# Kernel optimization log

Hardware: AMD Instinct MI355X
Metric: run time of the kernel (lower is better)

The kernel has to match this reference:

```python
import jax, jax.numpy as jnp
import numpy as np

# Config mirroring My_MLP(mlp_layers=2, isize=512, k=30, non_linearity='relu',
#                        mlp_act='relu', offset_list=[2048]*4)
SIZES = [2048, 2048, 2048, 2048]   # per-client subgraph sizes (offset_list)
N = sum(SIZES)                      # 8192 total nodes
D = 512                             # isize
K = 30 + 1                          # module uses self.k + 1


def setup_inputs() -> dict:
    key = jax.random.key(0)
    k1, k2, k3 = jax.random.split(key, 3)
    features = jax.random.normal(k1, (N, D), dtype=jnp.float32)
    # Diag layer weights: a learned diagonal (vector) per layer, init near 1.
    w0 = 1.0 + 0.1 * jax.random.normal(k2, (D,), dtype=jnp.float32)
    w1 = 1.0 + 0.1 * jax.random.normal(k3, (D,), dtype=jnp.float32)
    return {"features": features, "w0": w0, "w1": w1}


def reference(features, w0, w1):
    # internal_forward: Diag -> relu -> Diag (no act after last layer)
    h = jax.nn.relu(features * w0) * w1                 # [N, D]
    # F.normalize(dim=1, p=2)
    emb = h * jax.lax.rsqrt(jnp.sum(h * h, axis=1, keepdims=True) + 1e-24)
    sim = jnp.matmul(emb, emb.T)                        # [N, N]

    # cross_subgraph_topk: per row, keep top-(k+1) similarities among columns
    # belonging to a DIFFERENT client subgraph; zero everything else.
    seg = jnp.asarray(np.repeat(np.arange(len(SIZES)), SIZES))   # [N] int
    same = seg[:, None] == seg[None, :]                           # [N, N] bool
    masked = jnp.where(same, -jnp.inf, sim)
    vals, inds = jax.lax.top_k(masked, K)                         # [N, K]
    rows = jnp.arange(N)[:, None]
    out = jnp.zeros_like(sim).at[rows, inds].set(vals)

    # apply_non_linearity('relu', i)
    return jax.nn.relu(out)
```

## Files before the change

kernel.cpp:

```cpp
#include <hip/hip_runtime.h>
#include <hip/hip_bf16.h>
#include <hip/hip_fp16.h>
#include <math.h>

typedef unsigned short u16;
typedef unsigned int u32;
typedef unsigned long long u64;
typedef __attribute__((ext_vector_type(8))) short bf16x8;
typedef __attribute__((ext_vector_type(4))) float f32x4;

#define N_NODES 8192
#define DIM 512
#define KSEL 31
#define BANDCAP 128
#define SEG_SIZE 2048
#define NVALID 6144
#define BAND_ULP 8

__device__ __forceinline__ u32 f16key(u32 h) {
  return (h & 0x8000u) ? (0xFFFFu & ~h) : (h | 0x8000u);
}
__device__ __forceinline__ u32 packkeys(u32 w) {
  return f16key(w & 0xFFFFu) | (f16key(w >> 16) << 16);
}
__device__ __forceinline__ float keyval(u32 k) {
  const u16 raw = (k & 0x8000u) ? (u16)(k ^ 0x8000u) : (u16)(~k & 0xFFFFu);
  __half_raw hr; hr.x = raw;
  return __half2float(__half(hr));
}

#define GLD_LDS16(g, l)                                        \
  __builtin_amdgcn_global_load_lds(                            \
      (const __attribute__((address_space(1))) void*)(g),      \
      (__attribute__((address_space(3))) void*)(l), 16, 0, 0)

__global__ __launch_bounds__(256) void prep_kernel(
    const float* __restrict__ feat, const float* __restrict__ w0,
    const float* __restrict__ w1, u16* __restrict__ embh,
    float* __restrict__ embf, u32* __restrict__ kmax32) {
#pragma clang fp contract(off)
  const int row = blockIdx.x;
  const int t = threadIdx.x;
  __shared__ float hs[DIM];
  __shared__ float partial[32];
  __shared__ float rinv_sh;

  const float2 x = *reinterpret_cast<const float2*>(feat + (size_t)row * DIM + t * 2);
  const float2 a = *reinterpret_cast<const float2*>(w0 + t * 2);
  const float2 b = *reinterpret_cast<const float2*>(w1 + t * 2);
  const float h0 = fmaxf(x.x * a.x, 0.0f) * b.x;
  const float h1 = fmaxf(x.y * a.y, 0.0f) * b.y;
  hs[t * 2] = h0;
  hs[t * 2 + 1] = h1;
  if (t == 0) kmax32[row] = 0u;
  __syncthreads();

  if (t < 32) {
    const int base = (t >> 3) * 128 + (t & 7);
    float v = hs[base];
    float acc = v * v;
    for (int i = 1; i < 16; ++i) {
      v = hs[base + 8 * i];
      const float vv = v * v;
      acc = acc + vv;
    }
    partial[t] = acc;
  }
  __syncthreads();
  if (t == 0) {
    float B[4];
    for (int blk = 0; blk < 4; ++blk) {
      const float* p = &partial[blk * 8];
      B[blk] = ((p[0] + p[1]) + (p[2] + p[3])) + ((p[4] + p[5]) + (p[6] + p[7]));
    }
    const float s = (B[0] + B[1]) + (B[2] + B[3]);
    const float sp = s + 1e-24f;
    const float qf = (float)sqrt((double)sp);
    rinv_sh = (float)(1.0 / (double)qf);
  }
  __syncthreads();
  const float rinv = rinv_sh;
  const float e0 = h0 * rinv;
  const float e1 = h1 * rinv;
  *reinterpret_cast<float2*>(embf + (size_t)row * DIM + t * 2) = make_float2(e0, e1);
  __hip_bfloat162 bb;
  bb.x = __float2bfloat16(e0);
  bb.y = __float2bfloat16(e1);
  *reinterpret_cast<__hip_bfloat162*>(embh + (size_t)row * DIM + t * 2) = bb;
}

__global__ __launch_bounds__(256) void gemm_kernel(const u16* __restrict__ embh,
                                                   __half* __restrict__ simh,
                                                   u32* __restrict__ kmax32) {
  __shared__ u16 As[128][64];
  __shared__ u16 Bs[128][64];
  const int tid = threadIdx.x;
  const int lane = tid & 63;
  const int wave = tid >> 6;
  const int wm = wave >> 1;
  const int wn = wave & 1;
  const int rowTile = blockIdx.y;
  const int segTileBase = (rowTile >> 4) << 4;
  const int cT = blockIdx.x;
  const int colTile = cT < segTileBase ? cT : cT + 16;
  const int row0 = rowTile * 128;
  const int col0 = colTile * 128;

  f32x4 acc[4][4] = {};

  for (int k0 = 0; k0 < DIM; k0 += 64) {
#pragma unroll
    for (int i = 0; i < 4; ++i) {
      const int flat = i * 256 + tid;
      const int r = flat >> 3;
      const int c = (flat & 7) * 8;
      GLD_LDS16(embh + (size_t)(row0 + r) * DIM + k0 + c, &As[r][c]);
      GLD_LDS16(embh + (size_t)(col0 + r) * DIM + k0 + c, &Bs[r][c]);
    }
    __syncthreads();
#pragma unroll
    for (int kk = 0; kk < 2; ++kk) {
      bf16x8 afr[4], bfr[4];
      const int koff = kk * 32 + (lane >> 4) * 8;
      const int rsel = lane & 15;
#pragma unroll
      for (int m = 0; m < 4; ++m)
        afr[m] = *reinterpret_cast<const bf16x8*>(&As[wm * 64 + m * 16 + rsel][koff]);
#pragma unroll
      for (int n = 0; n < 4; ++n)
        bfr[n] = *reinterpret_cast<const bf16x8*>(&Bs[wn * 64 + n * 16 + rsel][koff]);
#pragma unroll
      for (int m = 0; m < 4; ++m)
#pragma unroll
        for (int n = 0; n < 4; ++n)
          acc[m][n] = __builtin_amdgcn_mfma_f32_16x16x32_bf16(afr[m], bfr[n],
                                                              acc[m][n], 0, 0, 0);
    }
    __syncthreads();
  }
#pragma unroll
  for (int m = 0; m < 4; ++m)
#pragma unroll
    for (int n = 0; n < 4; ++n)
#pragma unroll
      for (int j = 0; j < 4; ++j) {
        const int r = row0 + wm * 64 + m * 16 + (lane >> 4) * 4 + j;
        const int pcol = cT * 128 + wn * 64 + n * 16 + (lane & 15);
        simh[(size_t)r * NVALID + pcol] = __float2half(acc[m][n][j]);
      }
#pragma unroll
  for (int m = 0; m < 4; ++m) {
#pragma unroll
    for (int j = 0; j < 4; ++j) {
      float vmax = fmaxf(fmaxf(acc[m][0][j], acc[m][1][j]),
                         fmaxf(acc[m][2][j], acc[m][3][j]));
#pragma unroll
      for (int off = 1; off < 16; off <<= 1)
        vmax = fmaxf(vmax, __shfl_xor(vmax, off, 64));
      if ((lane & 15) == 0) {
        const int r = row0 + wm * 64 + m * 16 + (lane >> 4) * 4 + j;
        const u32 b = __float_as_uint(vmax);
        const u32 kk = (b & 0x80000000u) ? ~b : (b | 0x80000000u);
        atomicMax(&kmax32[r], kk);
      }
    }
  }
}

__global__ __launch_bounds__(256) void select_kernel(
    const __half* __restrict__ simh, const float* __restrict__ embf,
    const u32* __restrict__ kmax32, int2* __restrict__ compact) {
  const int row = blockIdx.x;
  const int t = threadIdx.x;
  const int lane = t & 63;
  const int wave = t >> 6;

  __shared__ u32 hist[257];
  __shared__ int bcol[BANDCAP];
  __shared__ float bex[BANDCAP];
  __shared__ int outidx_s[KSEL];
  __shared__ float outval_s[KSEL];
  __shared__ int cnts[2];
  __shared__ u32 sh_lo, sh_hi, sh_need;
  __shared__ int sh_state;

  const int segBase = (row >> 11) << 11;

  u32 pk[12];
  {
    const uint4* src = reinterpret_cast<const uint4*>(simh + (size_t)row * NVALID);
    const uint4 a = src[t], b = src[256 + t], c = src[512 + t];
    pk[0] = packkeys(a.x); pk[1] = packkeys(a.y);
    pk[2] = packkeys(a.z); pk[3] = packkeys(a.w);
    pk[4] = packkeys(b.x); pk[5] = packkeys(b.y);
    pk[6] = packkeys(b.z); pk[7] = packkeys(b.w);
    pk[8] = packkeys(c.x); pk[9] = packkeys(c.y);
    pk[10] = packkeys(c.z); pk[11] = packkeys(c.w);
  }
#define KEY(v) ((pk[(v) >> 1] >> (((v) & 1) * 16)) & 0xFFFFu)
#define COL(v) ((((((v) >> 3) * 256) + t) << 3) + ((v) & 7))

  if (t < KSEL) { outidx_s[t] = segBase; outval_s[t] = 0.0f; }
  if (t == 0) { cnts[0] = 0; cnts[1] = 0; }

  u32 kmax16;
  {
    const u32 kk = kmax32[row];
    const u32 fb = (kk & 0x80000000u) ? (kk ^ 0x80000000u) : ~kk;
    const __half h = __float2half(__uint_as_float(fb));
    kmax16 = f16key((u32)__half_as_ushort(h));
  }

  u32 base = (kmax16 > 511u) ? kmax16 - 511u : 0u;
  u32 winTop = kmax16;
  u32 shift = 2;
  u32 need = KSEL;
  int tier = 0;
  for (int guard = 0; guard < 6; ++guard) {
    hist[t] = 0;
    if (t == 0) hist[256] = 0;
    __syncthreads();
#pragma unroll
    for (int v = 0; v < 24; ++v) {
      const u32 k = KEY(v);
      if (k >= base && k <= winTop) atomicAdd(&hist[(k - base) >> shift], 1u);
    }
    __syncthreads();
    if (wave == 0) {
      const int x = lane * 4;
      const u32 b0 = hist[x], b1 = hist[x + 1];
      const u32 b2 = hist[x + 2], b3 = hist[x + 3];
      const u32 tot = b0 + b1 + b2 + b3;
      u32 inc = tot;
#pragma unroll
      for (int off = 1; off < 64; off <<= 1) {
        const u32 vv = (u32)__shfl_down((int)inc, off, 64);
        if (lane + off < 64) inc += vv;
      }
      const u32 exc = inc - tot;
      const u32 g3 = exc, g2 = g3 + b3, g1 = g2 + b2, g0 = g1 + b1;
      int sel = -1;
      u32 gsel = 0;
      if (g3 < need && g3 + b3 >= need) { sel = x + 3; gsel = g3; }
      else if (g2 < need && g2 + b2 >= need) { sel = x + 2; gsel = g2; }
      else if (g1 < need && g1 + b1 >= need) { sel = x + 1; gsel = g1; }
      else if (g0 < need && g0 + b0 >= need) { sel = x;     gsel = g0; }
      const u64 bal = __ballot(sel >= 0);
      if (lane == 0 && bal == 0) sh_state = 0;
      if (bal != 0) {
        const int srcl = (int)(__ffsll((unsigned long long)bal) - 1);
        sel  = __shfl(sel, srcl, 64);
        gsel = (u32)__shfl((int)gsel, srcl, 64);
        if (lane == 0) {
          const u32 blo = base + ((u32)sel << shift);
          const u32 bhi = min(blo + (1u << shift) - 1u, winTop);
          sh_lo = blo; sh_hi = bhi; sh_need = need - gsel;
          sh_state = (shift > 2) ? 1 : 2;
        }
      }
    }
    __syncthreads();
    const int st = sh_state;
    if (st == 2) break;
    if (st == 1) {
      base = sh_lo; winTop = sh_hi; shift = 0; need = sh_need;
    } else {
      ++tier;
      if (tier == 1) { base = (kmax16 > 8191u) ? kmax16 - 8191u : 0u; shift = 5; }
      else { base = 0u; shift = 8; }
      winTop = kmax16; need = KSEL;
    }
    __syncthreads();
  }
  const u32 binlo = sh_lo, binhi = sh_hi;
  const u32 hiK = binhi + BAND_ULP;
  const u32 loK = (binlo >= BAND_ULP) ? binlo - BAND_ULP : 0u;

#pragma unroll
  for (int v = 0; v < 24; ++v) {
    const u32 k = KEY(v);
    if (k > hiK) {
      const int slot = atomicAdd(&cnts[1], 1);
      const int i = COL(v);
      if (slot < KSEL) {
        outidx_s[slot] = (i < segBase) ? i : i + SEG_SIZE;
        outval_s[slot] = fmaxf(keyval(k), 0.0f);
      }
    } else if (k >= loK) {
      const int slot = atomicAdd(&cnts[0], 1);
      const int i = COL(v);
      if (slot < BANDCAP) bcol[slot] = (i < segBase) ? i : i + SEG_SIZE;
    }
  }
  __syncthreads();
  const int nH = min(cnts[1], KSEL);
  const int slots = KSEL - nH;
  const int nB = min(cnts[0], BANDCAP);

  if (t < nB) {
#pragma clang fp contract(off)
    const float4* g4 =
        reinterpret_cast<const float4*>(embf + (size_t)bcol[t] * DIM);
    const float4* e4 = reinterpret_cast<const float4*>(embf + (size_t)row * DIM);
    float acc = 0.0f;
    for (int k4 = 0; k4 < DIM / 4; ++k4) {
      const float4 a = e4[k4];
      const float4 b = g4[k4];
      acc = acc + a.x * b.x;
      acc = acc + a.y * b.y;
      acc = acc + a.z * b.z;
      acc = acc + a.w * b.w;
    }
    bex[t] = acc;
  }
  __syncthreads();

  if (t < nB) {
    const float ev = bex[t];
    const int ec = bcol[t];
    int r = 0;
    for (int j = 0; j < nB; ++j) {
      const float oj = bex[j];
      const int cj = bcol[j];
      if (oj > ev || (oj == ev && cj < ec)) r++;
    }
    if (r < slots) {
      const int slot = atomicAdd(&cnts[1], 1);
      if (slot < KSEL) { outidx_s[slot] = ec; outval_s[slot] = fmaxf(ev, 0.0f); }
    }
  }
  __syncthreads();
  if (t < KSEL)
    compact[(size_t)row * KSEL + t] =
        make_int2(outidx_s[t], __float_as_int(outval_s[t]));
#undef KEY
#undef COL
}

__global__ __launch_bounds__(256) void write_kernel(
    const int2* __restrict__ compact, float* __restrict__ out) {
  const int row = blockIdx.x;
  const int t = threadIdx.x;
  __shared__ int sidx[KSEL];
  __shared__ float sval[KSEL];
  if (t < KSEL) {
    const int2 e = compact[(size_t)row * KSEL + t];
    sidx[t] = e.x;
    sval[t] = __int_as_float(e.y);
  }
  float* orow = out + (size_t)row * N_NODES;
  const float4 zero4 = make_float4(0.f, 0.f, 0.f, 0.f);
  __syncthreads();
#pragma unroll
  for (int i = 0; i < 8; ++i)
    reinterpret_cast<float4*>(orow)[i * 256 + t] = zero4;
  __syncthreads();
  if (t < KSEL) orow[sidx[t]] = sval[t];
}

extern "C" void kernel_launch(void* const* d_in, const int* in_sizes, int n_in,
                              void* d_out, int out_size, void* d_ws, size_t ws_size,
                              hipStream_t stream) {
  const float* feat = (const float*)d_in[0];
  const float* w0 = (const float*)d_in[1];
  const float* w1 = (const float*)d_in[2];
  float* out = (float*)d_out;

  u16* embh = (u16*)d_ws;
  float* embf = (float*)((char*)d_ws + (size_t)N_NODES * DIM * 2);
  u32* kmax32 = (u32*)((char*)d_ws + (size_t)24 * 1024 * 1024);
  int2* compact = (int2*)d_ws;
  __half* simh = (__half*)d_out;

  prep_kernel<<<N_NODES, 256, 0, stream>>>(feat, w0, w1, embh, embf, kmax32);
  dim3 grid(48, 64);
  gemm_kernel<<<grid, 256, 0, stream>>>(embh, simh, kmax32);
  select_kernel<<<N_NODES, 256, 0, stream>>>(simh, embf, kmax32, compact);
  write_kernel<<<N_NODES, 256, 0, stream>>>(compact, out);
}
```

Baseline: 246.3 us.

## Fuse top-k selection with output write using workspace for fp16 similarity

The fp16 similarity matrix moves out of the output buffer into the workspace when the workspace is large enough. Selection can then zero and scatter the output rows directly, so the separate write kernel and the compact buffer round trip are no longer needed. Each select block now handles four rows in sequence, giving 2048 blocks instead of 8192. This depends on the workspace size at run time and falls back to the old two-kernel path otherwise. Fewer blocks may reduce latency hiding in the histogram and selection phases.

After: 265.4 us. 1.08x slower.

```diff
diff --git a/kernel.cpp b/kernel.cpp
--- a/kernel.cpp
+++ b/kernel.cpp
@@ -167,10 +167,11 @@
   }
 }
 
+template <bool FUSED>
 __global__ __launch_bounds__(256) void select_kernel(
     const __half* __restrict__ simh, const float* __restrict__ embf,
-    const u32* __restrict__ kmax32, int2* __restrict__ compact) {
-  const int row = blockIdx.x;
+    const u32* __restrict__ kmax32, int2* __restrict__ compact,
+    float* __restrict__ out) {
   const int t = threadIdx.x;
   const int lane = t & 63;
   const int wave = t >> 6;
@@ -184,157 +185,172 @@
   __shared__ u32 sh_lo, sh_hi, sh_need;
   __shared__ int sh_state;
 
-  const int segBase = (row >> 11) << 11;
-
-  u32 pk[12];
-  {
-    const uint4* src = reinterpret_cast<const uint4*>(simh + (size_t)row * NVALID);
-    const uint4 a = src[t], b = src[256 + t], c = src[512 + t];
-    pk[0] = packkeys(a.x); pk[1] = packkeys(a.y);
-    pk[2] = packkeys(a.z); pk[3] = packkeys(a.w);
-    pk[4] = packkeys(b.x); pk[5] = packkeys(b.y);
-    pk[6] = packkeys(b.z); pk[7] = packkeys(b.w);
-    pk[8] = packkeys(c.x); pk[9] = packkeys(c.y);
-    pk[10] = packkeys(c.z); pk[11] = packkeys(c.w);
-  }
+  for (int rr = 0; rr < 4; ++rr) {
+    const int row = blockIdx.x * 4 + rr;
+    const int segBase = (row >> 11) << 11;
+
+    u32 pk[12];
+    {
+      const uint4* src = reinterpret_cast<const uint4*>(simh + (size_t)row * NVALID);
+      const uint4 a = src[t], b = src[256 + t], c = src[512 + t];
+      pk[0] = packkeys(a.x); pk[1] = packkeys(a.y);
+      pk[2] = packkeys(a.z); pk[3] = packkeys(a.w);
+      pk[4] = packkeys(b.x); pk[5] = packkeys(b.y);
+      pk[6] = packkeys(b.z); pk[7] = packkeys(b.w);
+      pk[8] = packkeys(c.x); pk[9] = packkeys(c.y);
+      pk[10] = packkeys(c.z); pk[11] = packkeys(c.w);
+    }
 #define KEY(v) ((pk[(v) >> 1] >> (((v) & 1) * 16)) & 0xFFFFu)
 #define COL(v) ((((((v) >> 3) * 256) + t) << 3) + ((v) & 7))
 
-  if (t < KSEL) { outidx_s[t] = segBase; outval_s[t] = 0.0f; }
-  if (t == 0) { cnts[0] = 0; cnts[1] = 0; }
-
-  u32 kmax16;
-  {
-    const u32 kk = kmax32[row];
-    const u32 fb = (kk & 0x80000000u) ? (kk ^ 0x80000000u) : ~kk;
-    const __half h = __float2half(__uint_as_float(fb));
-    kmax16 = f16key((u32)__half_as_ushort(h));
-  }
-
-  u32 base = (kmax16 > 511u) ? kmax16 - 511u : 0u;
-  u32 winTop = kmax16;
-  u32 shift = 2;
-  u32 need = KSEL;
-  int tier = 0;
-  for (int guard = 0; guard < 6; ++guard) {
-    hist[t] = 0;
-    if (t == 0) hist[256] = 0;
-    __syncthreads();
+    if (t < KSEL) { outidx_s[t] = segBase; outval_s[t] = 0.0f; }
+    if (t == 0) { cnts[0] = 0; cnts[1] = 0; }
+
+    u32 kmax16;
+    {
+      const u32 kk = kmax32[row];
+      const u32 fb = (kk & 0x80000000u) ? (kk ^ 0x80000000u) : ~kk;
+      const __half h = __float2half(__uint_as_float(fb));
+      kmax16 = f16key((u32)__half_as_ushort(h));
+    }
+
+    u32 base = (kmax16 > 511u) ? kmax16 - 511u : 0u;
+    u32 winTop = kmax16;
+    u32 shift = 2;
+    u32 need = KSEL;
+    int tier = 0;
+    for (int guard = 0; guard < 6; ++guard) {
+      hist[t] = 0;
+      if (t == 0) hist[256] = 0;
+      __syncthreads();
+#pragma unroll
+      for (int v = 0; v < 24; ++v) {
+        const u32 k = KEY(v);
+        if (k >= base && k <= winTop) atomicAdd(&hist[(k - base) >> shift], 1u);
+      }
+      __syncthreads();
+      if (wave == 0) {
+        const int x = lane * 4;
+        const u32 b0 = hist[x], b1 = hist[x + 1];
+        const u32 b2 = hist[x + 2], b3 = hist[x + 3];
+        const u32 tot = b0 + b1 + b2 + b3;
+        u32 inc = tot;
+#pragma unroll
+        for (int off = 1; off < 64; off <<= 1) {
+          const u32 vv = (u32)__shfl_down((int)inc, off, 64);
+          if (lane + off < 64) inc += vv;
+        }
+        const u32 exc = inc - tot;
+        const u32 g3 = exc, g2 = g3 + b3, g1 = g2 + b2, g0 = g1 + b1;
+        int sel = -1;
+        u32 gsel = 0;
+        if (g3 < need && g3 + b3 >= need) { sel = x + 3; gsel = g3; }
+        else if (g2 < need && g2 + b2 >= need) { sel = x + 2; gsel = g2; }
+        else if (g1 < need && g1 + b1 >= need) { sel = x + 1; gsel = g1; }
+        else if (g0 < need && g0 + b0 >= need) { sel = x;     gsel = g0; }
+        const u64 bal = __ballot(sel >= 0);
+        if (lane == 0 && bal == 0) sh_state = 0;
+        if (bal != 0) {
+          const int srcl = (int)(__ffsll((unsigned long long)bal) - 1);
+          sel  = __shfl(sel, srcl, 64);
+          gsel = (u32)__shfl((int)gsel, srcl, 64);
+          if (lane == 0) {
+            const u32 blo = base + ((u32)sel << shift);
+            const u32 bhi = min(blo + (1u << shift) - 1u, winTop);
+            sh_lo = blo; sh_hi = bhi; sh_need = need - gsel;
+            sh_state = (shift > 2) ? 1 : 2;
+          }
+        }
+      }
+      __syncthreads();
+      const int st = sh_state;
+      if (st == 2) break;
+      if (st == 1) {
+        base = sh_lo; winTop = sh_hi; shift = 0; need = sh_need;
+      } else {
+        ++tier;
+        if (tier == 1) { base = (kmax16 > 8191u) ? kmax16 - 8191u : 0u; shift = 5; }
+        else { base = 0u; shift = 8; }
+        winTop = kmax16; need = KSEL;
+      }
+      __syncthreads();
+    }
+    const u32 binlo = sh_lo, binhi = sh_hi;
+    const u32 hiK = binhi + BAND_ULP;
+    const u32 loK = (binlo >= BAND_ULP) ? binlo - BAND_ULP : 0u;
+
 #pragma unroll
     for (int v = 0; v < 24; ++v) {
       const u32 k = KEY(v);
-      if (k >= base && k <= winTop) atomicAdd(&hist[(k - base) >> shift], 1u);
-    }
-    __syncthreads();
-    if (wave == 0) {
-      const int x = lane * 4;
-      const u32 b0 = hist[x], b1 = hist[x + 1];
-      const u32 b2 = hist[x + 2], b3 = hist[x + 3];
-      const u32 tot = b0 + b1 + b2 + b3;
-      u32 inc = tot;
-#pragma unroll
-      for (int off = 1; off < 64; off <<= 1) {
-        const u32 vv = (u32)__shfl_down((int)inc, off, 64);
-        if (lane + off < 64) inc += vv;
-      }
-      const u32 exc = inc - tot;
-      const u32 g3 = exc, g2 = g3 + b3, g1 = g2 + b2, g0 = g1 + b1;
-      int sel = -1;
-      u32 gsel = 0;
-      if (g3 < need && g3 + b3 >= need) { sel = x + 3; gsel = g3; }
-      else if (g2 < need && g2 + b2 >= need) { sel = x + 2; gsel = g2; }
-      else if (g1 < need && g1 + b1 >= need) { sel = x + 1; gsel = g1; }
-      else if (g0 < need && g0 + b0 >= need) { sel = x;     gsel = g0; }
-      const u64 bal = __ballot(sel >= 0);
-      if (lane == 0 && bal == 0) sh_state = 0;
-      if (bal != 0) {
-        const int srcl = (int)(__ffsll((unsigned long long)bal) - 1);
-        sel  = __shfl(sel, srcl, 64);
-        gsel = (u32)__shfl((int)gsel, srcl, 64);
-        if (lane == 0) {
-          const u32 blo = base + ((u32)sel << shift);
-          const u32 bhi = min(blo + (1u << shift) - 1u, winTop);
-          sh_lo = blo; sh_hi = bhi; sh_need = need - gsel;
-          sh_state = (shift > 2) ? 1 : 2;
+      if (k > hiK) {
+        const int slot = atomicAdd(&cnts[1], 1);
+        const int i = COL(v);
+        if (slot < KSEL) {
+          outidx_s[slot] = (i < segBase) ? i : i + SEG_SIZE;
+          outval_s[slot] = fmaxf(keyval(k), 0.0f);
         }
-      }
-    }
-    __syncthreads();
-    const int st = sh_state;
-    if (st == 2) break;
-    if (st == 1) {
-      base = sh_lo; winTop = sh_hi; shift = 0; need = sh_need;
+      } else if (k >= loK) {
+        const int slot = atomicAdd(&cnts[0], 1);
+        const int i = COL(v);
+        if (slot < BANDCAP) bcol[slot] = (i < segBase) ? i : i + SEG_SIZE;
+      }
+    }
+    __syncthreads();
+    const int nH = min(cnts[1], KSEL);
+    const int slots = KSEL - nH;
+    const int nB = min(cnts[0], BANDCAP);
+
+    if (t < nB) {
+#pragma clang fp contract(off)
+      const float4* g4 =
+          reinterpret_cast<const float4*>(embf + (size_t)bcol[t] * DIM);
+      const float4* e4 = reinterpret_cast<const float4*>(embf + (size_t)row * DIM);
+      float acc = 0.0f;
+      for (int k4 = 0; k4 < DIM / 4; ++k4) {
+        const float4 a = e4[k4];
+        const float4 b = g4[k4];
+        acc = acc + a.x * b.x;
+        acc = acc + a.y * b.y;
+        acc = acc + a.z * b.z;
+        acc = acc + a.w * b.w;
+      }
+      bex[t] = acc;
+    }
+    __syncthreads();
+
+    if (t < nB) {
+      const float ev = bex[t];
+      const int ec = bcol[t];
+      int r = 0;
+      for (int j = 0; j < nB; ++j) {
+        const float oj = bex[j];
+        const int cj = bcol[j];
+        if (oj > ev || (oj == ev && cj < ec)) r++;
+      }
+      if (r < slots) {
+        const int slot = atomicAdd(&cnts[1], 1);
+        if (slot < KSEL) { outidx_s[slot] = ec; outval_s[slot] = fmaxf(ev, 0.0f); }
+      }
+    }
+    __syncthreads();
+
+    if constexpr (FUSED) {
+      float* orow = out + (size_t)row * N_NODES;
+      const float4 zero4 = make_float4(0.f, 0.f, 0.f, 0.f);
+#pragma unroll
+      for (int i = 0; i < 8; ++i)
+        reinterpret_cast<float4*>(orow)[i * 256 + t] = zero4;
+      __syncthreads();
+      if (t < KSEL) orow[outidx_s[t]] = outval_s[t];
     } else {
-      ++tier;
-      if (tier == 1) { base = (kmax16 > 8191u) ? kmax16 - 8191u : 0u; shift = 5; }
-      else { base = 0u; shift = 8; }
-      winTop = kmax16; need = KSEL;
-    }
-    __syncthreads();
-  }
-  const u32 binlo = sh_lo, binhi = sh_hi;
-  const u32 hiK = binhi + BAND_ULP;
-  const u32 loK = (binlo >= BAND_ULP) ? binlo - BAND_ULP : 0u;
-
-#pragma unroll
-  for (int v = 0; v < 24; ++v) {
-    const u32 k = KEY(v);
-    if (k > hiK) {
-      const int slot = atomicAdd(&cnts[1], 1);
-      const int i = COL(v);
-      if (slot < KSEL) {
-        outidx_s[slot] = (i < segBase) ? i : i + SEG_SIZE;
-        outval_s[slot] = fmaxf(keyval(k), 0.0f);
-      }
-    } else if (k >= loK) {
-      const int slot = atomicAdd(&cnts[0], 1);
-      const int i = COL(v);
-      if (slot < BANDCAP) bcol[slot] = (i < segBase) ? i : i + SEG_SIZE;
-    }
-  }
-  __syncthreads();
-  const int nH = min(cnts[1], KSEL);
-  const int slots = KSEL - nH;
-  const int nB = min(cnts[0], BANDCAP);
-
-  if (t < nB) {
-#pragma clang fp contract(off)
-    const float4* g4 =
-        reinterpret_cast<const float4*>(embf + (size_t)bcol[t] * DIM);
-    const float4* e4 = reinterpret_cast<const float4*>(embf + (size_t)row * DIM);
-    float acc = 0.0f;
-    for (int k4 = 0; k4 < DIM / 4; ++k4) {
-      const float4 a = e4[k4];
-      const float4 b = g4[k4];
-      acc = acc + a.x * b.x;
-      acc = acc + a.y * b.y;
-      acc = acc + a.z * b.z;
-      acc = acc + a.w * b.w;
-    }
-    bex[t] = acc;
-  }
-  __syncthreads();
-
-  if (t < nB) {
-    const float ev = bex[t];
-    const int ec = bcol[t];
-    int r = 0;
-    for (int j = 0; j < nB; ++j) {
-      const float oj = bex[j];
-      const int cj = bcol[j];
-      if (oj > ev || (oj == ev && cj < ec)) r++;
-    }
-    if (r < slots) {
-      const int slot = atomicAdd(&cnts[1], 1);
-      if (slot < KSEL) { outidx_s[slot] = ec; outval_s[slot] = fmaxf(ev, 0.0f); }
-    }
-  }
-  __syncthreads();
-  if (t < KSEL)
-    compact[(size_t)row * KSEL + t] =
-        make_int2(outidx_s[t], __float_as_int(outval_s[t]));
+      if (t < KSEL)
+        compact[(size_t)row * KSEL + t] =
+            make_int2(outidx_s[t], __float_as_int(outval_s[t]));
+    }
+    __syncthreads();
 #undef KEY
 #undef COL
+  }
 }
 
 __global__ __launch_bounds__(256) void write_kernel(
@@ -370,11 +386,21 @@
   float* embf = (float*)((char*)d_ws + (size_t)N_NODES * DIM * 2);
   u32* kmax32 = (u32*)((char*)d_ws + (size_t)24 * 1024 * 1024);
   int2* compact = (int2*)d_ws;
-  __half* simh = (__half*)d_out;
+
+  const size_t simh_off = (size_t)32 * 1024 * 1024;
+  const size_t simh_bytes = (size_t)N_NODES * NVALID * 2;
+  const bool fused = ws_size >= simh_off + simh_bytes;
+  __half* simh = fused ? (__half*)((char*)d_ws + simh_off) : (__half*)d_out;
 
   prep_kernel<<<N_NODES, 256, 0, stream>>>(feat, w0, w1, embh, embf, kmax32);
   dim3 grid(48, 64);
   gemm_kernel<<<grid, 256, 0, stream>>>(embh, simh, kmax32);
-  select_kernel<<<N_NODES, 256, 0, stream>>>(simh, embf, kmax32, compact);
-  write_kernel<<<N_NODES, 256, 0, stream>>>(compact, out);
-}
+  if (fused) {
+    select_kernel<true><<<N_NODES / 4, 256, 0, stream>>>(simh, embf, kmax32,
+                                                         compact, out);
+  } else {
+    select_kernel<false><<<N_NODES / 4, 256, 0, stream>>>(simh, embf, kmax32,
+                                                          compact, out);
+    write_kernel<<<N_NODES, 256, 0, stream>>>(compact, out);
+  }
+}
```

## Exploit similarity symmetry in GEMM and shortcut band refinement in top-k select

Applied to the files above, without the earlier changes.

The GEMM now computes only tiles above the diagonal and writes each tile twice: once normally and once transposed into the mirrored rows of the fp16 similarity buffer. It also updates the per-row maxima for the mirrored rows, which roughly halves the MFMA work. The transposed stores are narrow strided writes, and the extra column-max atomics add traffic. The select kernel switches to a coarser histogram schedule with fewer refinement passes. When the boundary band exactly fills the remaining slots, it takes fp16 key values directly instead of recomputing fp32 dot products, which lowers the precision of those outputs.

New measurement: 225.9 us. 8.3% less time.

```diff
diff --git a/kernel.cpp b/kernel.cpp
--- a/kernel.cpp
+++ b/kernel.cpp
@@ -92,8 +92,6 @@
 __global__ __launch_bounds__(256) void gemm_kernel(const u16* __restrict__ embh,
                                                    __half* __restrict__ simh,
                                                    u32* __restrict__ kmax32) {
-  __shared__ u16 As[128][64];
-  __shared__ u16 Bs[128][64];
   const int tid = threadIdx.x;
   const int lane = tid & 63;
   const int wave = tid >> 6;
@@ -103,9 +101,12 @@
   const int segTileBase = (rowTile >> 4) << 4;
   const int cT = blockIdx.x;
   const int colTile = cT < segTileBase ? cT : cT + 16;
+  if (colTile <= rowTile) return;
   const int row0 = rowTile * 128;
   const int col0 = colTile * 128;
 
+  __shared__ u16 As[128][64];
+  __shared__ u16 Bs[128][64];
   f32x4 acc[4][4] = {};
 
   for (int k0 = 0; k0 < DIM; k0 += 64) {
@@ -138,6 +139,7 @@
     }
     __syncthreads();
   }
+
 #pragma unroll
   for (int m = 0; m < 4; ++m)
 #pragma unroll
@@ -148,6 +150,25 @@
         const int pcol = cT * 128 + wn * 64 + n * 16 + (lane & 15);
         simh[(size_t)r * NVALID + pcol] = __float2half(acc[m][n][j]);
       }
+  {
+    const int segBaseC = (col0 >> 11) << 11;
+    const int radj = (row0 < segBaseC) ? 0 : -SEG_SIZE;
+#pragma unroll
+    for (int m = 0; m < 4; ++m)
+#pragma unroll
+      for (int n = 0; n < 4; ++n) {
+        const int c = col0 + wn * 64 + n * 16 + (lane & 15);
+        const int rbase = row0 + wm * 64 + m * 16 + (lane >> 4) * 4;
+        const __half h0 = __float2half(acc[m][n][0]);
+        const __half h1 = __float2half(acc[m][n][1]);
+        const __half h2 = __float2half(acc[m][n][2]);
+        const __half h3 = __float2half(acc[m][n][3]);
+        uint2 pkd;
+        pkd.x = (u32)__half_as_ushort(h0) | ((u32)__half_as_ushort(h1) << 16);
+        pkd.y = (u32)__half_as_ushort(h2) | ((u32)__half_as_ushort(h3) << 16);
+        *reinterpret_cast<uint2*>(&simh[(size_t)c * NVALID + radj + rbase]) = pkd;
+      }
+  }
 #pragma unroll
   for (int m = 0; m < 4; ++m) {
 #pragma unroll
@@ -165,6 +186,22 @@
       }
     }
   }
+#pragma unroll
+  for (int n = 0; n < 4; ++n) {
+    float cmax = acc[0][n][0];
+#pragma unroll
+    for (int m = 0; m < 4; ++m)
+#pragma unroll
+      for (int j = 0; j < 4; ++j) cmax = fmaxf(cmax, acc[m][n][j]);
+    cmax = fmaxf(cmax, __shfl_xor(cmax, 16, 64));
+    cmax = fmaxf(cmax, __shfl_xor(cmax, 32, 64));
+    if ((lane >> 4) == 0) {
+      const int c = col0 + wn * 64 + n * 16 + (lane & 15);
+      const u32 b = __float_as_uint(cmax);
+      const u32 kk = (b & 0x80000000u) ? ~b : (b | 0x80000000u);
+      atomicMax(&kmax32[c], kk);
+    }
+  }
 }
 
 __global__ __launch_bounds__(256) void select_kernel(
@@ -177,6 +214,7 @@
 
   __shared__ u32 hist[257];
   __shared__ int bcol[BANDCAP];
+  __shared__ u32 bkey[BANDCAP];
   __shared__ float bex[BANDCAP];
   __shared__ int outidx_s[KSEL];
   __shared__ float outval_s[KSEL];
@@ -211,12 +249,11 @@
     kmax16 = f16key((u32)__half_as_ushort(h));
   }
 
-  u32 base = (kmax16 > 511u) ? kmax16 - 511u : 0u;
+  u32 base = (kmax16 > 4095u) ? kmax16 - 4095u : 0u;
   u32 winTop = kmax16;
-  u32 shift = 2;
+  u32 shift = 4;
   u32 need = KSEL;
-  int tier = 0;
-  for (int guard = 0; guard < 6; ++guard) {
+  for (int guard = 0; guard < 4; ++guard) {
     hist[t] = 0;
     if (t == 0) hist[256] = 0;
     __syncthreads();
@@ -255,7 +292,7 @@
           const u32 blo = base + ((u32)sel << shift);
           const u32 bhi = min(blo + (1u << shift) - 1u, winTop);
           sh_lo = blo; sh_hi = bhi; sh_need = need - gsel;
-          sh_state = (shift > 2) ? 1 : 2;
+          sh_state = (shift > 4) ? 1 : 2;
         }
       }
     }
@@ -263,12 +300,9 @@
     const int st = sh_state;
     if (st == 2) break;
     if (st == 1) {
-      base = sh_lo; winTop = sh_hi; shift = 0; need = sh_need;
+      base = sh_lo; winTop = sh_hi; shift = 4; need = sh_need;
     } else {
-      ++tier;
-      if (tier == 1) { base = (kmax16 > 8191u) ? kmax16 - 8191u : 0u; shift = 5; }
-      else { base = 0u; shift = 8; }
-      winTop = kmax16; need = KSEL;
+      base = 0u; winTop = kmax16; shift = 8; need = KSEL;
     }
     __syncthreads();
   }
@@ -289,7 +323,10 @@
     } else if (k >= loK) {
       const int slot = atomicAdd(&cnts[0], 1);
       const int i = COL(v);
-      if (slot < BANDCAP) bcol[slot] = (i < segBase) ? i : i + SEG_SIZE;
+      if (slot < BANDCAP) {
+        bcol[slot] = (i < segBase) ? i : i + SEG_SIZE;
+        bkey[slot] = k;
+      }
     }
   }
   __syncthreads();
@@ -297,36 +334,45 @@
   const int slots = KSEL - nH;
   const int nB = min(cnts[0], BANDCAP);
 
-  if (t < nB) {
+  if (nB == slots) {
+    if (t < nB) {
+      const int slot = atomicAdd(&cnts[1], 1);
+      if (slot < KSEL) {
+        outidx_s[slot] = bcol[t];
+        outval_s[slot] = fmaxf(keyval(bkey[t]), 0.0f);
+      }
+    }
+  } else {
+    if (t < nB) {
 #pragma clang fp contract(off)
-    const float4* g4 =
-        reinterpret_cast<const float4*>(embf + (size_t)bcol[t] * DIM);
-    const float4* e4 = reinterpret_cast<const float4*>(embf + (size_t)row * DIM);
-    float acc = 0.0f;
-    for (int k4 = 0; k4 < DIM / 4; ++k4) {
-      const float4 a = e4[k4];
-      const float4 b = g4[k4];
-      acc = acc + a.x * b.x;
-      acc = acc + a.y * b.y;
-      acc = acc + a.z * b.z;
-      acc = acc + a.w * b.w;
-    }
-    bex[t] = acc;
-  }
-  __syncthreads();
-
-  if (t < nB) {
-    const float ev = bex[t];
-    const int ec = bcol[t];
-    int r = 0;
-    for (int j = 0; j < nB; ++j) {
-      const float oj = bex[j];
-      const int cj = bcol[j];
-      if (oj > ev || (oj == ev && cj < ec)) r++;
-    }
-    if (r < slots) {
-      const int slot = atomicAdd(&cnts[1], 1);
-      if (slot < KSEL) { outidx_s[slot] = ec; outval_s[slot] = fmaxf(ev, 0.0f); }
+      const float4* g4 =
+          reinterpret_cast<const float4*>(embf + (size_t)bcol[t] * DIM);
+      const float4* e4 = reinterpret_cast<const float4*>(embf + (size_t)row * DIM);
+      float acc = 0.0f;
+      for (int k4 = 0; k4 < DIM / 4; ++k4) {
+        const float4 a = e4[k4];
+        const float4 b = g4[k4];
+        acc = acc + a.x * b.x;
+        acc = acc + a.y * b.y;
+        acc = acc + a.z * b.z;
+        acc = acc + a.w * b.w;
+      }
+      bex[t] = acc;
+    }
+    __syncthreads();
+    if (t < nB) {
+      const float ev = bex[t];
+      const int ec = bcol[t];
+      int r = 0;
+      for (int j = 0; j < nB; ++j) {
+        const float oj = bex[j];
+        const int cj = bcol[j];
+        if (oj > ev || (oj == ev && cj < ec)) r++;
+      }
+      if (r < slots) {
+        const int slot = atomicAdd(&cnts[1], 1);
+        if (slot < KSEL) { outidx_s[slot] = ec; outval_s[slot] = fmaxf(ev, 0.0f); }
+      }
     }
   }
   __syncthreads();
```
